# Optimization experiments

Measured on AMD Instinct MI355X. Metric: run time of the kernel, lower is better.

Reference implementation:

```python
import jax, jax.numpy as jnp
from jax import lax
import numpy as np

B, Q, C = 128, 200, 92  # batch, num_queries, num_classes (0 = no-object)


def hungarian(cost):
    """Exact Hungarian assignment (augmenting-path / JV potentials, e-maxx form).
    cost: [n, n]. Returns col_of_row: [n] int32, the column matched to each row.
    Uses 1-based columns/rows internally; index 0 is the sentinel."""
    n = cost.shape[0]
    INF = jnp.asarray(1e9, cost.dtype)

    def solve_row(i, carry):
        u, v, p = carry
        p = p.at[0].set(jnp.int32(i))
        minv = jnp.full(n + 1, INF, cost.dtype)
        way = jnp.zeros(n + 1, jnp.int32)
        used = jnp.zeros(n + 1, bool)
        state = (u, v, p, minv, way, used, jnp.int32(0))

        def cond(s):
            _u, _v, _p, _minv, _way, _used, j0 = s
            return _p[j0] != 0

        def body(s):
            u, v, p, minv, way, used, j0 = s
            used = used.at[j0].set(True)
            i0 = p[j0]
            cur = cost[i0 - 1, :] - u[i0] - v[1:]          # reduced costs of row i0
            cur = jnp.where(used[1:], INF, cur)
            upd = cur < minv[1:]
            minv = minv.at[1:].set(jnp.where(upd, cur, minv[1:]))
            way = way.at[1:].set(jnp.where(upd, j0, way[1:]))
            masked = jnp.where(used[1:], INF, minv[1:])
            j1 = jnp.argmin(masked).astype(jnp.int32) + 1
            delta = masked[j1 - 1]
            zero = jnp.asarray(0, cost.dtype)
            u = u.at[p].add(jnp.where(used, delta, zero))  # u[p[j]] += delta for used j (rows distinct)
            v = jnp.where(used, v - delta, v)
            minv = jnp.where(used, minv, minv - delta)
            return (u, v, p, minv, way, used, j1)

        u, v, p, minv, way, used, j0 = lax.while_loop(cond, body, state)

        def aug_body(s):  # flip matching along the alternating path
            p, j0 = s
            j1 = way[j0]
            return p.at[j0].set(p[j1]), j1

        p, _ = lax.while_loop(lambda s: s[1] != 0, aug_body, (p, j0))
        return (u, v, p)

    u0 = jnp.zeros(n + 1, cost.dtype)
    v0 = jnp.zeros(n + 1, cost.dtype)
    p0 = jnp.zeros(n + 1, jnp.int32)
    _, _, p = lax.fori_loop(1, n + 1, solve_row, (u0, v0, p0))
    # p[j] = row matched to column j (1-based); invert to col per row (0-based)
    col_of_row = jnp.zeros(n, jnp.int32).at[p[1:] - 1].set(jnp.arange(n, dtype=jnp.int32))
    return col_of_row


def cost_matrix(pred_cat, pred_bbox, tar_cat, tar_bbox):
    b, q, c = pred_cat.shape
    log_probs = jax.nn.log_softmax(pred_cat, axis=-1)                  # [B,Qp,C]
    idx = jnp.broadcast_to(tar_cat[:, None, :], (b, q, q))             # [B,Qp,Qt]
    ce = -jnp.take_along_axis(log_probs, idx, axis=2)                  # CE(pred_i, tgt_j)
    d = pred_bbox[:, :, None, :] - tar_bbox[:, None, :, :]             # [B,Qp,Qt,4]
    ad = jnp.abs(d)
    sl1 = jnp.where(ad < 1.0, 0.5 * d * d, ad - 0.5).sum(-1)           # SmoothL1 (beta=1)
    mask = (tar_cat != 0).astype(sl1.dtype)[:, None, :]                # bbox loss only for real objects
    return ce + sl1 * mask                                             # [B,Qp,Qt]


def setup_inputs() -> dict:
    key = jax.random.key(0)
    k1, k2, k3, k4 = jax.random.split(key, 4)
    pred_cat = jax.random.normal(k1, (B, Q, C), dtype=jnp.float32)
    pred_bbox = jax.random.uniform(k2, (B, Q, 4), dtype=jnp.float32)
    tar_cat = jax.random.randint(k3, (B, Q), 0, C, dtype=jnp.int32)
    tar_bbox = jax.random.uniform(k4, (B, Q, 4), dtype=jnp.float32)
    return {"pred_cat": pred_cat, "pred_bbox": pred_bbox, "tar_cat": tar_cat, "tar_bbox": tar_bbox}


def reference(pred_cat, pred_bbox, tar_cat, tar_bbox):
    cost = cost_matrix(pred_cat, pred_bbox, tar_cat, tar_bbox)         # [B,Q,Q]
    col = jax.vmap(hungarian)(lax.stop_gradient(cost))                 # assignment on detached cost
    out = jnp.take_along_axis(cost, col[:, :, None], axis=2)[..., 0]   # [B,Q] per-query matched loss
    return out
```

## Files before the change

### kernel.cpp

```cpp
#include <hip/hip_runtime.h>
#include <math.h>

#define BB 128
#define QQ 200
#define CC 92
#define CMPAD (QQ * QQ + 64)

__global__ void lse_kernel(const float* __restrict__ pc, float* __restrict__ lse) {
    int idx = blockIdx.x * blockDim.x + threadIdx.x;
    if (idx >= BB * QQ) return;
    const float* row = pc + (size_t)idx * CC;
    float m = -INFINITY;
    for (int c = 0; c < CC; ++c) m = fmaxf(m, row[c]);
    float s = 0.f;
    for (int c = 0; c < CC; ++c) s += expf(row[c] - m);
    lse[idx] = m + logf(s);
}

__global__ void cost_kernel(const float* __restrict__ pc,
                            const float* __restrict__ pb,
                            const int*   __restrict__ tc,
                            const float* __restrict__ tb,
                            const float* __restrict__ lse,
                            float* __restrict__ cost) {
    long idx = blockIdx.x * (long)blockDim.x + threadIdx.x;
    if (idx >= (long)BB * QQ * QQ) return;
    int j = (int)(idx % QQ);
    int i = (int)((idx / QQ) % QQ);
    int b = (int)(idx / ((long)QQ * QQ));
    int cls = tc[b * QQ + j];
    float ce = lse[b * QQ + i] - pc[((size_t)(b * QQ + i)) * CC + cls];
    const float* pbb = pb + ((size_t)(b * QQ + i)) * 4;
    const float* tbb = tb + ((size_t)(b * QQ + j)) * 4;
    float sl1 = 0.f;
#pragma unroll
    for (int k = 0; k < 4; ++k) {
        float d = pbb[k] - tbb[k];
        float ad = fabsf(d);
        sl1 += (ad < 1.f) ? 0.5f * d * d : (ad - 0.5f);
    }
    float mask = (cls != 0) ? 1.f : 0.f;
    cost[idx] = ce + sl1 * mask;
}

__device__ __forceinline__ int rdlane_i(int x, int l) { return __builtin_amdgcn_readlane(x, l); }
__device__ __forceinline__ float rdlane_f(float x, int l) {
    return __uint_as_float((unsigned)__builtin_amdgcn_readlane((int)__float_as_uint(x), l));
}

__device__ __forceinline__ float wave_fmin_bcast(float x) {
    float y;
#define DPPSTEP(ctrl) \
    y = __uint_as_float((unsigned)__builtin_amdgcn_update_dpp( \
            (int)__float_as_uint(x), (int)__float_as_uint(x), ctrl, 0xf, 0xf, false)); \
    x = fminf(x, y);
    DPPSTEP(0x111) DPPSTEP(0x112) DPPSTEP(0x114) DPPSTEP(0x118)
    DPPSTEP(0x142) DPPSTEP(0x143)
#undef DPPSTEP
    return rdlane_f(x, 63);
}

__global__ __launch_bounds__(64) void hungarian_kernel(const float* __restrict__ cost,
                                                       float* __restrict__ out) {
    const int b = blockIdx.x;
    const int t = threadIdx.x;
    const float* cb = cost + (size_t)b * QQ * QQ;

    __shared__ __align__(16) float cm[CMPAD];

    {
        const float4* src = (const float4*)cb;
        float4* dst = (float4*)cm;
        for (int idx = t; idx < QQ * QQ / 4; idx += 64) dst[idx] = src[idx];
    }

    const float INF = 1e9f;
    const int nval = (t < 8) ? 4 : 3;

    float v[4]     = {0.f, 0.f, 0.f, 0.f};
    int   pslot[4] = {0, 0, 0, 0};
    float uslot[4] = {0.f, 0.f, 0.f, 0.f};
    float minv[4];
    int   waysl[4];
    int   usedm;
    float usent;

    for (int i = 1; i <= QQ; ++i) {
        minv[0] = minv[1] = minv[2] = minv[3] = INF;
        waysl[0] = waysl[1] = waysl[2] = waysl[3] = 0;
        usedm = 0;
        usent = 0.f;
        int j0 = 0;
        float u0 = 0.f;
        const float* crow = cm + (i - 1) * QQ;
        float c0 = crow[t];
        float c1 = crow[64 + t];
        float c2 = crow[128 + t];
        float c3 = crow[192 + t];

        for (;;) {
            if (j0 > 0) {
                int s = (j0 - 1) >> 6;
                if (((j0 - 1) & 63) == t) usedm |= 1 << s;
            }

            float kv0, kv1, kv2, kv3;
            {
                float cur;
                cur = c0 - u0 - v[0];
                if (!(usedm & 1) && cur < minv[0]) { minv[0] = cur; waysl[0] = j0; }
                kv0 = (usedm & 1) ? INF : minv[0];
                cur = c1 - u0 - v[1];
                if (!(usedm & 2) && cur < minv[1]) { minv[1] = cur; waysl[1] = j0; }
                kv1 = (usedm & 2) ? INF : minv[1];
                cur = c2 - u0 - v[2];
                if (!(usedm & 4) && cur < minv[2]) { minv[2] = cur; waysl[2] = j0; }
                kv2 = (usedm & 4) ? INF : minv[2];
                cur = c3 - u0 - v[3];
                if (!(usedm & 8) && t < 8 && cur < minv[3]) { minv[3] = cur; waysl[3] = j0; }
                kv3 = ((usedm & 8) || t >= 8) ? INF : minv[3];
            }

            float gmin = wave_fmin_bcast(fminf(fminf(kv0, kv1), fminf(kv2, kv3)));
            float delta = gmin;

            unsigned long long m0 = __ballot(kv0 == gmin);
            unsigned long long m1 = __ballot(kv1 == gmin);
            unsigned long long m2 = __ballot(kv2 == gmin);
            unsigned long long m3 = __ballot(kv3 == gmin);
            int j1;
            if (m0)      j1 = 1   + (int)__builtin_ctzll(m0);
            else if (m1) j1 = 65  + (int)__builtin_ctzll(m1);
            else if (m2) j1 = 129 + (int)__builtin_ctzll(m2);
            else         j1 = 193 + (int)__builtin_ctzll(m3);

            int kk = (j1 - 1) >> 6, ln = (j1 - 1) & 63;
            int   ps = (kk == 0) ? pslot[0] : (kk == 1) ? pslot[1]
                      : (kk == 2) ? pslot[2] : pslot[3];
            float us = (kk == 0) ? uslot[0] : (kk == 1) ? uslot[1]
                      : (kk == 2) ? uslot[2] : uslot[3];
            int pi = rdlane_i(ps, ln);

            int nr = (pi > 0 ? pi : 1) - 1;
            const float* nrow = cm + nr * QQ;
            float n0 = nrow[t];
            float n1 = nrow[64 + t];
            float n2 = nrow[128 + t];
            float n3 = nrow[192 + t];

            float u0n = rdlane_f(us, ln);

#pragma unroll
            for (int k = 0; k < 4; ++k) {
                if (usedm & (1 << k)) {
                    v[k] -= delta;
                    uslot[k] += delta;
                } else if (k < nval) {
                    minv[k] -= delta;
                }
            }
            usent += delta;

            if (pi == 0) { j0 = j1; break; }
            j0 = j1; u0 = u0n;
            c0 = n0; c1 = n1; c2 = n2; c3 = n3;
        }

        {
            int jj = j0;
            while (jj != 0) {
                int jm = jj - 1, km = jm >> 6, lm = jm & 63;
                int ws = (km == 0) ? waysl[0] : (km == 1) ? waysl[1]
                        : (km == 2) ? waysl[2] : waysl[3];
                int jn = rdlane_i(ws, lm);
                int pnew; float unew;
                if (jn == 0) {
                    pnew = i;
                    unew = usent;
                } else {
                    int jm2 = jn - 1, kn = jm2 >> 6, ln2 = jm2 & 63;
                    int   ps2 = (kn == 0) ? pslot[0] : (kn == 1) ? pslot[1]
                               : (kn == 2) ? pslot[2] : pslot[3];
                    float us2 = (kn == 0) ? uslot[0] : (kn == 1) ? uslot[1]
                               : (kn == 2) ? uslot[2] : uslot[3];
                    pnew = rdlane_i(ps2, ln2);
                    unew = rdlane_f(us2, ln2);
                }
                if (lm == t) { pslot[km] = pnew; uslot[km] = unew; }
                jj = jn;
            }
        }
    }

#pragma unroll
    for (int k = 0; k < 4; ++k) {
        if (k < nval) {
            int jc = 1 + t + 64 * k;
            int row = pslot[k] - 1;
            out[b * QQ + row] = cm[row * QQ + (jc - 1)];
        }
    }
}

extern "C" void kernel_launch(void* const* d_in, const int* in_sizes, int n_in,
                              void* d_out, int out_size, void* d_ws, size_t ws_size,
                              hipStream_t stream) {
    const float* pred_cat  = (const float*)d_in[0];
    const float* pred_bbox = (const float*)d_in[1];
    const int*   tar_cat   = (const int*)d_in[2];
    const float* tar_bbox  = (const float*)d_in[3];
    float* out = (float*)d_out;

    float* cost = (float*)d_ws;
    float* lse  = cost + (size_t)BB * QQ * QQ;

    lse_kernel<<<(BB * QQ + 255) / 256, 256, 0, stream>>>(pred_cat, lse);
    cost_kernel<<<((long)BB * QQ * QQ + 255) / 256, 256, 0, stream>>>(
        pred_cat, pred_bbox, tar_cat, tar_bbox, lse, cost);
    hungarian_kernel<<<BB, 64, 0, stream>>>(cost, out);
}
```

Measured before the change: 1.463 ms.

## Remap columns to 4-per-lane layout and shorten argmin dependency chain

Columns are reassigned so each of the first 50 lanes owns four consecutive columns, and the shared-memory cost rows are permuted so each lane's four entries sit at stride 50. The argmin now uses one ballot plus readlanes of the winning lane's local column, row and potential instead of four ballots and a column-indexed lookup. A precomputed running minimum of the masked minv values is carried across iterations, so the wave reduction no longer waits for the minv update. The minv/way updates are moved after the reduction to overlap with the next row load. Lanes 50-63 sit idle, and the extra bookkeeping adds some register pressure.

```diff
diff --git a/kernel.cpp b/kernel.cpp
--- a/kernel.cpp
+++ b/kernel.cpp
@@ -4,7 +4,7 @@
 #define BB 128
 #define QQ 200
 #define CC 92
-#define CMPAD (QQ * QQ + 64)
+#define CMPAD (QQ * QQ + 80)
 
 __global__ void lse_kernel(const float* __restrict__ pc, float* __restrict__ lse) {
     int idx = blockIdx.x * blockDim.x + threadIdx.x;
@@ -70,98 +70,105 @@
 
     {
         const float4* src = (const float4*)cb;
-        float4* dst = (float4*)cm;
-        for (int idx = t; idx < QQ * QQ / 4; idx += 64) dst[idx] = src[idx];
+        for (int idx = t; idx < QQ * QQ / 4; idx += 64) {
+            int i  = idx / 50;
+            int c4 = idx % 50;
+            float4 val = src[idx];
+            float* rowp = cm + i * QQ;
+            rowp[c4]        = val.x;
+            rowp[50 + c4]   = val.y;
+            rowp[100 + c4]  = val.z;
+            rowp[150 + c4]  = val.w;
+        }
     }
 
     const float INF = 1e9f;
-    const int nval = (t < 8) ? 4 : 3;
 
     float v[4]     = {0.f, 0.f, 0.f, 0.f};
     int   pslot[4] = {0, 0, 0, 0};
     float uslot[4] = {0.f, 0.f, 0.f, 0.f};
     float minv[4];
+    float mminv[4];
     int   waysl[4];
     int   usedm;
     float usent;
 
     for (int i = 1; i <= QQ; ++i) {
         minv[0] = minv[1] = minv[2] = minv[3] = INF;
+        mminv[0] = mminv[1] = mminv[2] = mminv[3] = INF;
         waysl[0] = waysl[1] = waysl[2] = waysl[3] = 0;
-        usedm = 0;
+        usedm = (t < 50) ? 0 : 0xF;
         usent = 0.f;
+        float premin = INF;
         int j0 = 0;
         float u0 = 0.f;
         const float* crow = cm + (i - 1) * QQ;
         float c0 = crow[t];
-        float c1 = crow[64 + t];
-        float c2 = crow[128 + t];
-        float c3 = crow[192 + t];
+        float c1 = crow[50 + t];
+        float c2 = crow[100 + t];
+        float c3 = crow[150 + t];
 
         for (;;) {
-            if (j0 > 0) {
-                int s = (j0 - 1) >> 6;
-                if (((j0 - 1) & 63) == t) usedm |= 1 << s;
-            }
-
-            float kv0, kv1, kv2, kv3;
-            {
-                float cur;
-                cur = c0 - u0 - v[0];
-                if (!(usedm & 1) && cur < minv[0]) { minv[0] = cur; waysl[0] = j0; }
-                kv0 = (usedm & 1) ? INF : minv[0];
-                cur = c1 - u0 - v[1];
-                if (!(usedm & 2) && cur < minv[1]) { minv[1] = cur; waysl[1] = j0; }
-                kv1 = (usedm & 2) ? INF : minv[1];
-                cur = c2 - u0 - v[2];
-                if (!(usedm & 4) && cur < minv[2]) { minv[2] = cur; waysl[2] = j0; }
-                kv2 = (usedm & 4) ? INF : minv[2];
-                cur = c3 - u0 - v[3];
-                if (!(usedm & 8) && t < 8 && cur < minv[3]) { minv[3] = cur; waysl[3] = j0; }
-                kv3 = ((usedm & 8) || t >= 8) ? INF : minv[3];
-            }
-
-            float gmin = wave_fmin_bcast(fminf(fminf(kv0, kv1), fminf(kv2, kv3)));
+            float cur0 = (c0 - u0) - v[0];
+            float cur1 = (c1 - u0) - v[1];
+            float cur2 = (c2 - u0) - v[2];
+            float cur3 = (c3 - u0) - v[3];
+            float m0 = (usedm & 1) ? INF : cur0;
+            float m1 = (usedm & 2) ? INF : cur1;
+            float m2 = (usedm & 4) ? INF : cur2;
+            float m3 = (usedm & 8) ? INF : cur3;
+            float x = fminf(fminf(fminf(m0, m1), fminf(m2, m3)), premin);
+            float gmin = wave_fmin_bcast(x);
             float delta = gmin;
 
-            unsigned long long m0 = __ballot(kv0 == gmin);
-            unsigned long long m1 = __ballot(kv1 == gmin);
-            unsigned long long m2 = __ballot(kv2 == gmin);
-            unsigned long long m3 = __ballot(kv3 == gmin);
-            int j1;
-            if (m0)      j1 = 1   + (int)__builtin_ctzll(m0);
-            else if (m1) j1 = 65  + (int)__builtin_ctzll(m1);
-            else if (m2) j1 = 129 + (int)__builtin_ctzll(m2);
-            else         j1 = 193 + (int)__builtin_ctzll(m3);
-
-            int kk = (j1 - 1) >> 6, ln = (j1 - 1) & 63;
-            int   ps = (kk == 0) ? pslot[0] : (kk == 1) ? pslot[1]
-                      : (kk == 2) ? pslot[2] : pslot[3];
-            float us = (kk == 0) ? uslot[0] : (kk == 1) ? uslot[1]
-                      : (kk == 2) ? uslot[2] : uslot[3];
-            int pi = rdlane_i(ps, ln);
+            float kv0 = fminf(m0, mminv[0]);
+            float kv1 = fminf(m1, mminv[1]);
+            float kv2 = fminf(m2, mminv[2]);
+            float kv3 = fminf(m3, mminv[3]);
+            int lk = (kv0 == gmin) ? 0 : (kv1 == gmin) ? 1 : (kv2 == gmin) ? 2 : 3;
+            int   cj = 4 * t + lk + 1;
+            int   cp = (lk == 0) ? pslot[0] : (lk == 1) ? pslot[1]
+                      : (lk == 2) ? pslot[2] : pslot[3];
+            float cu = (lk == 0) ? uslot[0] : (lk == 1) ? uslot[1]
+                      : (lk == 2) ? uslot[2] : uslot[3];
+
+            unsigned long long mm = __ballot(x == gmin);
+            int ts = (int)__builtin_ctzll(mm);
+            int   j1  = rdlane_i(cj, ts);
+            int   pi  = rdlane_i(cp, ts);
+            float u0n = rdlane_f(cu, ts);
 
             int nr = (pi > 0 ? pi : 1) - 1;
             const float* nrow = cm + nr * QQ;
             float n0 = nrow[t];
-            float n1 = nrow[64 + t];
-            float n2 = nrow[128 + t];
-            float n3 = nrow[192 + t];
-
-            float u0n = rdlane_f(us, ln);
-
+            float n1 = nrow[50 + t];
+            float n2 = nrow[100 + t];
+            float n3 = nrow[150 + t];
+
+            if (!(usedm & 1) && cur0 < minv[0]) { minv[0] = cur0; waysl[0] = j0; }
+            if (!(usedm & 2) && cur1 < minv[1]) { minv[1] = cur1; waysl[1] = j0; }
+            if (!(usedm & 4) && cur2 < minv[2]) { minv[2] = cur2; waysl[2] = j0; }
+            if (!(usedm & 8) && cur3 < minv[3]) { minv[3] = cur3; waysl[3] = j0; }
 #pragma unroll
             for (int k = 0; k < 4; ++k) {
                 if (usedm & (1 << k)) {
                     v[k] -= delta;
                     uslot[k] += delta;
-                } else if (k < nval) {
+                } else {
                     minv[k] -= delta;
                 }
             }
             usent += delta;
 
             if (pi == 0) { j0 = j1; break; }
+
+            if (t == ts) usedm |= 1 << lk;
+            mminv[0] = (usedm & 1) ? INF : minv[0];
+            mminv[1] = (usedm & 2) ? INF : minv[1];
+            mminv[2] = (usedm & 4) ? INF : minv[2];
+            mminv[3] = (usedm & 8) ? INF : minv[3];
+            premin = fminf(fminf(mminv[0], mminv[1]), fminf(mminv[2], mminv[3]));
+
             j0 = j1; u0 = u0n;
             c0 = n0; c1 = n1; c2 = n2; c3 = n3;
         }
@@ -169,35 +176,34 @@
         {
             int jj = j0;
             while (jj != 0) {
-                int jm = jj - 1, km = jm >> 6, lm = jm & 63;
-                int ws = (km == 0) ? waysl[0] : (km == 1) ? waysl[1]
-                        : (km == 2) ? waysl[2] : waysl[3];
+                int jm = jj - 1, lm = jm >> 2, sm = jm & 3;
+                int ws = (sm == 0) ? waysl[0] : (sm == 1) ? waysl[1]
+                        : (sm == 2) ? waysl[2] : waysl[3];
                 int jn = rdlane_i(ws, lm);
                 int pnew; float unew;
                 if (jn == 0) {
                     pnew = i;
                     unew = usent;
                 } else {
-                    int jm2 = jn - 1, kn = jm2 >> 6, ln2 = jm2 & 63;
-                    int   ps2 = (kn == 0) ? pslot[0] : (kn == 1) ? pslot[1]
-                               : (kn == 2) ? pslot[2] : pslot[3];
-                    float us2 = (kn == 0) ? uslot[0] : (kn == 1) ? uslot[1]
-                               : (kn == 2) ? uslot[2] : uslot[3];
+                    int jm2 = jn - 1, ln2 = jm2 >> 2, sn = jm2 & 3;
+                    int   ps2 = (sn == 0) ? pslot[0] : (sn == 1) ? pslot[1]
+                               : (sn == 2) ? pslot[2] : pslot[3];
+                    float us2 = (sn == 0) ? uslot[0] : (sn == 1) ? uslot[1]
+                               : (sn == 2) ? uslot[2] : uslot[3];
                     pnew = rdlane_i(ps2, ln2);
                     unew = rdlane_f(us2, ln2);
                 }
-                if (lm == t) { pslot[km] = pnew; uslot[km] = unew; }
+                if (lm == t) { pslot[sm] = pnew; uslot[sm] = unew; }
                 jj = jn;
             }
         }
     }
 
+    if (t < 50) {
 #pragma unroll
-    for (int k = 0; k < 4; ++k) {
-        if (k < nval) {
-            int jc = 1 + t + 64 * k;
+        for (int k = 0; k < 4; ++k) {
             int row = pslot[k] - 1;
-            out[b * QQ + row] = cm[row * QQ + (jc - 1)];
+            out[b * QQ + row] = cm[row * QQ + 50 * k + t];
         }
     }
 }
```

Measured after the change: 1.839 ms. 1.26x slower.

## Defer Hungarian potential updates to end of each row search (Dijkstra-style distances)

Applied to the files above, without the earlier changes.

Reformulates the inner augmenting-path loop to track absolute shortest-path distances instead of updating minv, v and u by delta every iteration. Potentials for visited columns and rows are corrected once after the path is found, using the final distance minus each column's distance. Padding lanes are pre-marked as used so the t<8 checks drop out of the hot loop. This shortens the per-iteration serial dependency chain, but floating-point rounding differs from the incremental form and could change tie-breaking.

```diff
diff --git a/kernel.cpp b/kernel.cpp
--- a/kernel.cpp
+++ b/kernel.cpp
@@ -75,54 +75,49 @@
     }
 
     const float INF = 1e9f;
-    const int nval = (t < 8) ? 4 : 3;
+    const int nval  = (t < 8) ? 4 : 3;
+    const int initm = (t < 8) ? 0 : 8;
 
     float v[4]     = {0.f, 0.f, 0.f, 0.f};
     int   pslot[4] = {0, 0, 0, 0};
     float uslot[4] = {0.f, 0.f, 0.f, 0.f};
-    float minv[4];
-    int   waysl[4];
+    float d[4];
+    int   way[4];
     int   usedm;
-    float usent;
 
     for (int i = 1; i <= QQ; ++i) {
-        minv[0] = minv[1] = minv[2] = minv[3] = INF;
-        waysl[0] = waysl[1] = waysl[2] = waysl[3] = 0;
-        usedm = 0;
-        usent = 0.f;
+        d[0] = d[1] = d[2] = d[3] = INF;
+        way[0] = way[1] = way[2] = way[3] = 0;
+        usedm = initm;
+        float s = 0.f;
         int j0 = 0;
-        float u0 = 0.f;
         const float* crow = cm + (i - 1) * QQ;
         float c0 = crow[t];
         float c1 = crow[64 + t];
         float c2 = crow[128 + t];
         float c3 = crow[192 + t];
+        float muF;
 
         for (;;) {
             if (j0 > 0) {
-                int s = (j0 - 1) >> 6;
-                if (((j0 - 1) & 63) == t) usedm |= 1 << s;
+                int sl = (j0 - 1) >> 6;
+                if (((j0 - 1) & 63) == t) usedm |= 1 << sl;
             }
 
-            float kv0, kv1, kv2, kv3;
-            {
-                float cur;
-                cur = c0 - u0 - v[0];
-                if (!(usedm & 1) && cur < minv[0]) { minv[0] = cur; waysl[0] = j0; }
-                kv0 = (usedm & 1) ? INF : minv[0];
-                cur = c1 - u0 - v[1];
-                if (!(usedm & 2) && cur < minv[1]) { minv[1] = cur; waysl[1] = j0; }
-                kv1 = (usedm & 2) ? INF : minv[1];
-                cur = c2 - u0 - v[2];
-                if (!(usedm & 4) && cur < minv[2]) { minv[2] = cur; waysl[2] = j0; }
-                kv2 = (usedm & 4) ? INF : minv[2];
-                cur = c3 - u0 - v[3];
-                if (!(usedm & 8) && t < 8 && cur < minv[3]) { minv[3] = cur; waysl[3] = j0; }
-                kv3 = ((usedm & 8) || t >= 8) ? INF : minv[3];
-            }
+            float nd0 = (c0 + s) - v[0];
+            float nd1 = (c1 + s) - v[1];
+            float nd2 = (c2 + s) - v[2];
+            float nd3 = (c3 + s) - v[3];
+            if (!(usedm & 1) && nd0 < d[0]) { d[0] = nd0; way[0] = j0; }
+            if (!(usedm & 2) && nd1 < d[1]) { d[1] = nd1; way[1] = j0; }
+            if (!(usedm & 4) && nd2 < d[2]) { d[2] = nd2; way[2] = j0; }
+            if (!(usedm & 8) && nd3 < d[3]) { d[3] = nd3; way[3] = j0; }
+            float kv0 = (usedm & 1) ? INF : d[0];
+            float kv1 = (usedm & 2) ? INF : d[1];
+            float kv2 = (usedm & 4) ? INF : d[2];
+            float kv3 = (usedm & 8) ? INF : d[3];
 
             float gmin = wave_fmin_bcast(fminf(fminf(kv0, kv1), fminf(kv2, kv3)));
-            float delta = gmin;
 
             unsigned long long m0 = __ballot(kv0 == gmin);
             unsigned long long m1 = __ballot(kv1 == gmin);
@@ -150,28 +145,28 @@
 
             float u0n = rdlane_f(us, ln);
 
-#pragma unroll
-            for (int k = 0; k < 4; ++k) {
-                if (usedm & (1 << k)) {
-                    v[k] -= delta;
-                    uslot[k] += delta;
-                } else if (k < nval) {
-                    minv[k] -= delta;
-                }
-            }
-            usent += delta;
-
-            if (pi == 0) { j0 = j1; break; }
-            j0 = j1; u0 = u0n;
+            if (pi == 0) { j0 = j1; muF = gmin; break; }
+
+            s = gmin - u0n;
+            j0 = j1;
             c0 = n0; c1 = n1; c2 = n2; c3 = n3;
         }
+
+        {
+            int pu = usedm & ~initm;
+            if (pu & 1) { float a = muF - d[0]; v[0] -= a; uslot[0] += a; }
+            if (pu & 2) { float a = muF - d[1]; v[1] -= a; uslot[1] += a; }
+            if (pu & 4) { float a = muF - d[2]; v[2] -= a; uslot[2] += a; }
+            if (pu & 8) { float a = muF - d[3]; v[3] -= a; uslot[3] += a; }
+        }
+        float usent = muF;
 
         {
             int jj = j0;
             while (jj != 0) {
                 int jm = jj - 1, km = jm >> 6, lm = jm & 63;
-                int ws = (km == 0) ? waysl[0] : (km == 1) ? waysl[1]
-                        : (km == 2) ? waysl[2] : waysl[3];
+                int ws = (km == 0) ? way[0] : (km == 1) ? way[1]
+                        : (km == 2) ? way[2] : way[3];
                 int jn = rdlane_i(ws, lm);
                 int pnew; float unew;
                 if (jn == 0) {
```

After: 1.608 ms. +10.0%, slower.

## Shorten Hungarian critical path and restructure cost kernel to row-per-block

Applied to the files above, without the earlier changes.

The Hungarian inner loop now computes the min candidate with fminf before updating minv/way, moving the stateful updates off the reduction critical path. The used-mask update is deferred to the end of the iteration, and padding lanes are pre-marked as used so the per-slot t<8 checks are dropped. The cost kernel launches one block per (row, batch) with vectorized float4 box loads and no 64-bit div/mod indexing. Together these aim to cut serial latency per augmenting step in the dominant single-wave kernel, at the cost of some wasted threads (256 threads for 200 columns) in the cost kernel.

```diff
diff --git a/kernel.cpp b/kernel.cpp
--- a/kernel.cpp
+++ b/kernel.cpp
@@ -17,30 +17,33 @@
     lse[idx] = m + logf(s);
 }
 
-__global__ void cost_kernel(const float* __restrict__ pc,
-                            const float* __restrict__ pb,
-                            const int*   __restrict__ tc,
-                            const float* __restrict__ tb,
-                            const float* __restrict__ lse,
-                            float* __restrict__ cost) {
-    long idx = blockIdx.x * (long)blockDim.x + threadIdx.x;
-    if (idx >= (long)BB * QQ * QQ) return;
-    int j = (int)(idx % QQ);
-    int i = (int)((idx / QQ) % QQ);
-    int b = (int)(idx / ((long)QQ * QQ));
-    int cls = tc[b * QQ + j];
-    float ce = lse[b * QQ + i] - pc[((size_t)(b * QQ + i)) * CC + cls];
-    const float* pbb = pb + ((size_t)(b * QQ + i)) * 4;
-    const float* tbb = tb + ((size_t)(b * QQ + j)) * 4;
+__global__ __launch_bounds__(256) void cost_kernel2(const float* __restrict__ pc,
+                                                    const float* __restrict__ pb,
+                                                    const int*   __restrict__ tc,
+                                                    const float* __restrict__ tb,
+                                                    const float* __restrict__ lse,
+                                                    float* __restrict__ cost) {
+    const int i = blockIdx.x;
+    const int b = blockIdx.y;
+    const int j = threadIdx.x;
+    if (j >= QQ) return;
+    const int base = b * QQ;
+    const float l = lse[base + i];
+    const float* pcrow = pc + (size_t)(base + i) * CC;
+    const float4 pbb = *(const float4*)(pb + (size_t)(base + i) * 4);
+    const int cls = tc[base + j];
+    const float ce = l - pcrow[cls];
+    const float4 tbb = *(const float4*)(tb + (size_t)(base + j) * 4);
     float sl1 = 0.f;
-#pragma unroll
-    for (int k = 0; k < 4; ++k) {
-        float d = pbb[k] - tbb[k];
-        float ad = fabsf(d);
-        sl1 += (ad < 1.f) ? 0.5f * d * d : (ad - 0.5f);
-    }
-    float mask = (cls != 0) ? 1.f : 0.f;
-    cost[idx] = ce + sl1 * mask;
+    {
+        float d, ad;
+        d = pbb.x - tbb.x; ad = fabsf(d); sl1 += (ad < 1.f) ? 0.5f * d * d : (ad - 0.5f);
+        d = pbb.y - tbb.y; ad = fabsf(d); sl1 += (ad < 1.f) ? 0.5f * d * d : (ad - 0.5f);
+        d = pbb.z - tbb.z; ad = fabsf(d); sl1 += (ad < 1.f) ? 0.5f * d * d : (ad - 0.5f);
+        d = pbb.w - tbb.w; ad = fabsf(d); sl1 += (ad < 1.f) ? 0.5f * d * d : (ad - 0.5f);
+    }
+    const float mask = (cls != 0) ? 1.f : 0.f;
+    cost[(size_t)(base + i) * QQ + j] = ce + sl1 * mask;
 }
 
 __device__ __forceinline__ int rdlane_i(int x, int l) { return __builtin_amdgcn_readlane(x, l); }
@@ -75,7 +78,8 @@
     }
 
     const float INF = 1e9f;
-    const int nval = (t < 8) ? 4 : 3;
+    const int nval  = (t < 8) ? 4 : 3;
+    const int initm = (t < 8) ? 0 : 8;
 
     float v[4]     = {0.f, 0.f, 0.f, 0.f};
     int   pslot[4] = {0, 0, 0, 0};
@@ -88,7 +92,7 @@
     for (int i = 1; i <= QQ; ++i) {
         minv[0] = minv[1] = minv[2] = minv[3] = INF;
         waysl[0] = waysl[1] = waysl[2] = waysl[3] = 0;
-        usedm = 0;
+        usedm = initm;
         usent = 0.f;
         int j0 = 0;
         float u0 = 0.f;
@@ -99,28 +103,14 @@
         float c3 = crow[192 + t];
 
         for (;;) {
-            if (j0 > 0) {
-                int s = (j0 - 1) >> 6;
-                if (((j0 - 1) & 63) == t) usedm |= 1 << s;
-            }
-
-            float kv0, kv1, kv2, kv3;
-            {
-                float cur;
-                cur = c0 - u0 - v[0];
-                if (!(usedm & 1) && cur < minv[0]) { minv[0] = cur; waysl[0] = j0; }
-                kv0 = (usedm & 1) ? INF : minv[0];
-                cur = c1 - u0 - v[1];
-                if (!(usedm & 2) && cur < minv[1]) { minv[1] = cur; waysl[1] = j0; }
-                kv1 = (usedm & 2) ? INF : minv[1];
-                cur = c2 - u0 - v[2];
-                if (!(usedm & 4) && cur < minv[2]) { minv[2] = cur; waysl[2] = j0; }
-                kv2 = (usedm & 4) ? INF : minv[2];
-                cur = c3 - u0 - v[3];
-                if (!(usedm & 8) && t < 8 && cur < minv[3]) { minv[3] = cur; waysl[3] = j0; }
-                kv3 = ((usedm & 8) || t >= 8) ? INF : minv[3];
-            }
-
+            float cur0 = (c0 - u0) - v[0];
+            float cur1 = (c1 - u0) - v[1];
+            float cur2 = (c2 - u0) - v[2];
+            float cur3 = (c3 - u0) - v[3];
+            float kv0 = (usedm & 1) ? INF : fminf(minv[0], cur0);
+            float kv1 = (usedm & 2) ? INF : fminf(minv[1], cur1);
+            float kv2 = (usedm & 4) ? INF : fminf(minv[2], cur2);
+            float kv3 = (usedm & 8) ? INF : fminf(minv[3], cur3);
             float gmin = wave_fmin_bcast(fminf(fminf(kv0, kv1), fminf(kv2, kv3)));
             float delta = gmin;
 
@@ -150,18 +140,24 @@
 
             float u0n = rdlane_f(us, ln);
 
+            if (!(usedm & 1) && cur0 < minv[0]) { minv[0] = cur0; waysl[0] = j0; }
+            if (!(usedm & 2) && cur1 < minv[1]) { minv[1] = cur1; waysl[1] = j0; }
+            if (!(usedm & 4) && cur2 < minv[2]) { minv[2] = cur2; waysl[2] = j0; }
+            if (!(usedm & 8) && cur3 < minv[3]) { minv[3] = cur3; waysl[3] = j0; }
 #pragma unroll
             for (int k = 0; k < 4; ++k) {
                 if (usedm & (1 << k)) {
                     v[k] -= delta;
                     uslot[k] += delta;
-                } else if (k < nval) {
+                } else {
                     minv[k] -= delta;
                 }
             }
             usent += delta;
 
             if (pi == 0) { j0 = j1; break; }
+
+            if (ln == t) usedm |= 1 << kk;
             j0 = j1; u0 = u0n;
             c0 = n0; c1 = n1; c2 = n2; c3 = n3;
         }
@@ -215,7 +211,7 @@
     float* lse  = cost + (size_t)BB * QQ * QQ;
 
     lse_kernel<<<(BB * QQ + 255) / 256, 256, 0, stream>>>(pred_cat, lse);
-    cost_kernel<<<((long)BB * QQ * QQ + 255) / 256, 256, 0, stream>>>(
+    cost_kernel2<<<dim3(QQ, BB), 256, 0, stream>>>(
         pred_cat, pred_bbox, tar_cat, tar_bbox, lse, cost);
     hungarian_kernel<<<BB, 64, 0, stream>>>(cost, out);
 }
```

After: 1.535 ms. +4.9%, slower.
